# Performance work log

Hardware: AMD Instinct MI355X
Metric: run time of the kernel (lower is better)

Reference implementation:

```python
import jax, jax.numpy as jnp
import numpy as np
from jax.scipy.stats import norm

N_TOK, D_MODEL, N_EXP, N_SEL = 16384, 4096, 16, 4
NOISE_EPS = 0.01
LOSS_LAMBDA = 0.01


def setup_inputs() -> dict:
    key = jax.random.key(0)
    kx, k1, k2, kn, kz = jax.random.split(key, 5)
    x = jax.random.normal(kx, (N_TOK, D_MODEL), dtype=jnp.float32)
    w1 = jax.random.normal(k1, (N_EXP, D_MODEL), dtype=jnp.float32) * 0.02
    w2 = jax.random.normal(k2, (N_EXP, N_EXP), dtype=jnp.float32) * 0.02
    wn = jax.random.normal(kn, (N_EXP, D_MODEL), dtype=jnp.float32) * 0.02
    noise = jax.random.normal(kz, (N_TOK, N_EXP), dtype=jnp.float32)
    return {"x": x, "w1": w1, "w2": w2, "wn": wn, "noise": noise}


def _cv_squared(v, eps=1e-10):
    # torch .var() is unbiased (ddof=1)
    return jnp.var(v, ddof=1) / (jnp.mean(v) ** 2 + eps)


def reference(x, w1, w2, wn, noise):
    # MLP gate: Linear(D->E, no bias) -> tanh -> Linear(E->E, no bias)
    logits_gate = jnp.einsum("te,fe->tf", jnp.tanh(jnp.einsum("td,ed->te", x, w1)), w2)
    noise_control = jax.nn.softplus(jnp.einsum("td,ed->te", x, wn)) + NOISE_EPS
    logits_noise = noise * noise_control
    logits = logits_gate + logits_noise  # [T, E]

    m = min(N_SEL + 1, N_EXP)  # k+1 values for threshold computation
    top_logits, top_indices = jax.lax.top_k(logits, m)  # [T, m]
    top_k_logits = top_logits[:, :N_SEL]
    top_k_indices = top_indices[:, :N_SEL]
    top_k_scores = jax.nn.softmax(top_k_logits, axis=1)  # [T, k]

    # importance: scatter top-k scores back to dense [T, E]
    rows = jnp.arange(N_TOK)[:, None]
    scores_filtered = jnp.zeros_like(logits).at[rows, top_k_indices].set(top_k_scores)
    importance = scores_filtered.sum(0)  # [E]

    # load: smooth estimator via Normal CDF (faithful to source, which
    # compares logits_noise against the in/out thresholds)
    threshold_if_in = top_logits[:, N_SEL:N_SEL + 1]       # (k+1)-th top value, [T,1]
    threshold_if_out = top_logits[:, N_SEL - 1:N_SEL]      # k-th top value, [T,1]
    is_in = logits_noise > threshold_if_in
    prob_if_in = norm.cdf((logits_gate - threshold_if_in) / noise_control)
    prob_if_out = norm.cdf((logits_gate - threshold_if_out) / noise_control)
    prob = jnp.where(is_in, prob_if_in, prob_if_out)
    load = prob.sum(0)  # [E]

    gate_loss = LOSS_LAMBDA * (_cv_squared(importance) + _cv_squared(load))
    return top_k_indices, top_k_scores, gate_loss
```

## Files before the change

kernel.cpp:

```cpp
#include <hip/hip_runtime.h>
#include <math.h>

#define N_TOK   16384
#define D_MODEL 4096
#define N_EXP   16
#define N_SEL   4
#define WELEM   (N_EXP * D_MODEL)

typedef __bf16 bf16x8 __attribute__((ext_vector_type(8)));
typedef float  f32x4  __attribute__((ext_vector_type(4)));

#define MFMA(a, b, c) __builtin_amdgcn_mfma_f32_16x16x32_bf16((a), (b), (c), 0, 0, 0)
#define AS1 __attribute__((address_space(1)))
#define AS3 __attribute__((address_space(3)))

__global__ __launch_bounds__(256) void wprep_kernel(const float* __restrict__ w1,
                                                    const float* __restrict__ wn,
                                                    __bf16* __restrict__ wbuf)
{
    const int i = blockIdx.x * 256 + threadIdx.x;
    {
        const float v = w1[i];
        const __bf16 h = (__bf16)v;  const float r1 = v - (float)h;
        const __bf16 m = (__bf16)r1; const float r2 = r1 - (float)m;
        wbuf[i] = h; wbuf[WELEM + i] = m; wbuf[2 * WELEM + i] = (__bf16)r2;
    }
    {
        const float v = wn[i];
        const __bf16 h = (__bf16)v;  const float r1 = v - (float)h;
        const __bf16 m = (__bf16)r1; const float r2 = r1 - (float)m;
        wbuf[3 * WELEM + i] = h; wbuf[4 * WELEM + i] = m; wbuf[5 * WELEM + i] = (__bf16)r2;
    }
}

__device__ __forceinline__ void stage_load(const float* __restrict__ x,
                                           float4* xs, int buf, int w, int l,
                                           int t0, int kbase)
{
    #pragma unroll
    for (int j = 0; j < 8; ++j) {
        const int tl     = j * 2 + (l >> 5);
        const int k4slot = l & 31;
        const int k4data = k4slot ^ tl;
        const float* g = x + (size_t)(t0 + w * 16 + tl) * D_MODEL + kbase + k4data * 4;
        float4* lbase = xs + buf * 2048 + w * 512 + j * 64;
        __builtin_amdgcn_global_load_lds((const AS1 void*)(const void*)g,
                                         (AS3 void*)(void*)lbase, 16, 0, 0);
    }
}

__device__ __forceinline__ void split3(const float4 a, const float4 b,
                                       bf16x8& h, bf16x8& m, bf16x8& lo)
{
    const float v[8] = {a.x, a.y, a.z, a.w, b.x, b.y, b.z, b.w};
    #pragma unroll
    for (int j = 0; j < 8; ++j) {
        const __bf16 hh = (__bf16)v[j]; const float r1 = v[j] - (float)hh;
        const __bf16 mm = (__bf16)r1;   const float r2 = r1 - (float)mm;
        h[j] = hh; m[j] = mm; lo[j] = (__bf16)r2;
    }
}

__global__ __launch_bounds__(256, 2) void gate_kernel(
    const float* __restrict__ x, const __bf16* __restrict__ wbuf,
    const float* __restrict__ w2, const float* __restrict__ noise,
    float* __restrict__ out, float* __restrict__ g_imp, float* __restrict__ g_load)
{
    __shared__ float4 xs[4096];
    __shared__ float dsum[4][16][33];
    __shared__ float s_imp[N_EXP], s_ld[N_EXP];

    const int tid = threadIdx.x;
    const int l   = tid & 63;
    const int w   = tid >> 6;
    const int ml  = l & 15;
    const int q   = l >> 4;
    const int t0  = blockIdx.x * 64;

    const __bf16* w1h = wbuf;
    const __bf16* w1m = wbuf + WELEM;
    const __bf16* w1l = wbuf + 2 * WELEM;
    const __bf16* wnh = wbuf + 3 * WELEM;
    const __bf16* wnm = wbuf + 4 * WELEM;
    const __bf16* wnl = wbuf + 5 * WELEM;
    const int woff = ml * D_MODEL + q * 8;

    f32x4 c1 = {0.f, 0.f, 0.f, 0.f};
    f32x4 c2 = {0.f, 0.f, 0.f, 0.f};

    stage_load(x, xs, 0, w, l, t0, 0);
    if (tid < N_EXP) { s_imp[tid] = 0.f; s_ld[tid] = 0.f; }
    __syncthreads();

    for (int s = 0; s < 32; ++s) {
        if (s < 31) stage_load(x, xs, (s + 1) & 1, w, l, t0, (s + 1) * 128);

        const int kbase = s * 128;
        const int xb    = (s & 1) * 2048 + w * 512 + ml * 32;
        #pragma unroll
        for (int step = 0; step < 4; ++step) {
            const int kq = step * 8 + q * 2;
            const float4 va = xs[xb + (kq ^ ml)];
            const float4 vb = xs[xb + ((kq + 1) ^ ml)];
            bf16x8 xh, xm, xl;
            split3(va, vb, xh, xm, xl);

            const int wo = woff + kbase + step * 32;
            const bf16x8 a1h = *(const bf16x8*)(w1h + wo);
            const bf16x8 a1m = *(const bf16x8*)(w1m + wo);
            const bf16x8 a1l = *(const bf16x8*)(w1l + wo);
            const bf16x8 a2h = *(const bf16x8*)(wnh + wo);
            const bf16x8 a2m = *(const bf16x8*)(wnm + wo);
            const bf16x8 a2l = *(const bf16x8*)(wnl + wo);

            c1 = MFMA(a1h, xh, c1); c1 = MFMA(a1h, xm, c1); c1 = MFMA(a1m, xh, c1);
            c1 = MFMA(a1h, xl, c1); c1 = MFMA(a1l, xh, c1); c1 = MFMA(a1m, xm, c1);
            c2 = MFMA(a2h, xh, c2); c2 = MFMA(a2h, xm, c2); c2 = MFMA(a2m, xh, c2);
            c2 = MFMA(a2h, xl, c2); c2 = MFMA(a2l, xh, c2); c2 = MFMA(a2m, xm, c2);
        }
        __syncthreads();
    }

    #pragma unroll
    for (int r = 0; r < 4; ++r) {
        dsum[w][ml][q * 4 + r]      = c1[r];
        dsum[w][ml][16 + q * 4 + r] = c2[r];
    }
    __syncthreads();

    if (ml == l) {
        const int t = t0 + w * 16 + ml;
        float dot[32];
        #pragma unroll
        for (int e = 0; e < 32; ++e) dot[e] = dsum[w][ml][e];

        float th[N_EXP], nc[N_EXP];
        #pragma unroll
        for (int e = 0; e < N_EXP; ++e) th[e] = tanhf(dot[e]);
        #pragma unroll
        for (int e = 0; e < N_EXP; ++e) {
            const float v = dot[N_EXP + e];
            nc[e] = fmaxf(v, 0.f) + log1pf(expf(-fabsf(v))) + 0.01f;
        }

        float lg[N_EXP];
        #pragma unroll
        for (int f = 0; f < N_EXP; ++f) {
            float s = 0.f;
            #pragma unroll
            for (int e = 0; e < N_EXP; ++e) s = fmaf(th[e], w2[f * 16 + e], s);
            lg[f] = s;
        }

        float ln[N_EXP], v[N_EXP];
        {
            const float4* nz = (const float4*)(noise + (size_t)t * 16);
            const float4 n0 = nz[0], n1 = nz[1], n2 = nz[2], n3 = nz[3];
            const float nzv[16] = {n0.x, n0.y, n0.z, n0.w, n1.x, n1.y, n1.z, n1.w,
                                   n2.x, n2.y, n2.z, n2.w, n3.x, n3.y, n3.z, n3.w};
            #pragma unroll
            for (int e = 0; e < N_EXP; ++e) {
                ln[e] = nzv[e] * nc[e];
                v[e]  = lg[e] + ln[e];
            }
        }

        float tv[5]; int ti[5];
        #pragma unroll
        for (int j = 0; j < 5; ++j) {
            float best = -INFINITY; int bi = 0;
            #pragma unroll
            for (int e = 0; e < N_EXP; ++e) {
                bool taken = false;
                #pragma unroll
                for (int jj = 0; jj < 5; ++jj)
                    if (jj < j) taken = taken || (ti[jj] == e);
                if (!taken && v[e] > best) { best = v[e]; bi = e; }
            }
            tv[j] = best; ti[j] = bi;
        }

        const float mx = tv[0];
        float ex[4], ssum = 0.f;
        #pragma unroll
        for (int j = 0; j < 4; ++j) { ex[j] = expf(tv[j] - mx); ssum += ex[j]; }
        const float inv = 1.f / ssum;
        float sc[4];
        #pragma unroll
        for (int j = 0; j < 4; ++j) sc[j] = ex[j] * inv;

        #pragma unroll
        for (int j = 0; j < 4; ++j) atomicAdd(&s_imp[ti[j]], sc[j]);

        const float thr_in = tv[4], thr_out = tv[3];
        #pragma unroll
        for (int e = 0; e < N_EXP; ++e) {
            const bool  is_in = ln[e] > thr_in;
            const float thr   = is_in ? thr_in : thr_out;
            const float z     = (lg[e] - thr) / nc[e];
            const float prob  = 0.5f * (1.f + erff(z * 0.70710678118654752f));
            atomicAdd(&s_ld[e], prob);
        }

        ((float4*)out)[t] = make_float4((float)ti[0], (float)ti[1],
                                        (float)ti[2], (float)ti[3]);
        ((float4*)(out + N_TOK * N_SEL))[t] = make_float4(sc[0], sc[1], sc[2], sc[3]);
    }
    __syncthreads();
    if (tid < N_EXP)            atomicAdd(&g_imp[tid], s_imp[tid]);
    else if (tid < 2 * N_EXP)   atomicAdd(&g_load[tid - N_EXP], s_ld[tid - N_EXP]);
}

__global__ void loss_kernel(const float* __restrict__ g_imp,
                            const float* __restrict__ g_load,
                            float* __restrict__ out)
{
    if (threadIdx.x == 0 && blockIdx.x == 0) {
        double mi = 0.0, ml = 0.0;
        for (int e = 0; e < N_EXP; ++e) { mi += g_imp[e]; ml += g_load[e]; }
        mi /= N_EXP; ml /= N_EXP;
        double vi = 0.0, vl = 0.0;
        for (int e = 0; e < N_EXP; ++e) {
            const double di = g_imp[e] - mi;  vi += di * di;
            const double dl = g_load[e] - ml; vl += dl * dl;
        }
        vi /= (N_EXP - 1); vl /= (N_EXP - 1);
        const double ci = vi / (mi * mi + 1e-10);
        const double cl = vl / (ml * ml + 1e-10);
        out[N_TOK * N_SEL * 2] = (float)(0.01 * (ci + cl));
    }
}

extern "C" void kernel_launch(void* const* d_in, const int* in_sizes, int n_in,
                              void* d_out, int out_size, void* d_ws, size_t ws_size,
                              hipStream_t stream)
{
    const float* x     = (const float*)d_in[0];
    const float* w1    = (const float*)d_in[1];
    const float* w2    = (const float*)d_in[2];
    const float* wn    = (const float*)d_in[3];
    const float* noise = (const float*)d_in[4];
    float* out = (float*)d_out;

    __bf16* wbuf   = (__bf16*)d_ws;
    float*  g_imp  = (float*)((char*)d_ws + (1 << 20));
    float*  g_load = g_imp + N_EXP;

    hipMemsetAsync(g_imp, 0, 2 * N_EXP * sizeof(float), stream);

    wprep_kernel<<<WELEM / 256, 256, 0, stream>>>(w1, wn, wbuf);
    gate_kernel<<<N_TOK / 64, 256, 0, stream>>>(x, wbuf, w2, noise, out,
                                                g_imp, g_load);
    loss_kernel<<<1, 64, 0, stream>>>(g_imp, g_load, out);
}
```

Measured before the change: 457.1 us.

## Split-K the gate GEMM across blocks and move epilogue to separate kernel

```diff
diff --git a/kernel.cpp b/kernel.cpp
--- a/kernel.cpp
+++ b/kernel.cpp
@@ -6,13 +6,14 @@
 #define N_EXP   16
 #define N_SEL   4
 #define WELEM   (N_EXP * D_MODEL)
+#define KSPLIT  8
+#define KRANGE  (D_MODEL / KSPLIT)
+#define NSTEP   (KRANGE / 32)
 
 typedef __bf16 bf16x8 __attribute__((ext_vector_type(8)));
 typedef float  f32x4  __attribute__((ext_vector_type(4)));
 
 #define MFMA(a, b, c) __builtin_amdgcn_mfma_f32_16x16x32_bf16((a), (b), (c), 0, 0, 0)
-#define AS1 __attribute__((address_space(1)))
-#define AS3 __attribute__((address_space(3)))
 
 __global__ __launch_bounds__(256) void wprep_kernel(const float* __restrict__ w1,
                                                     const float* __restrict__ wn,
@@ -33,22 +34,6 @@
     }
 }
 
-__device__ __forceinline__ void stage_load(const float* __restrict__ x,
-                                           float4* xs, int buf, int w, int l,
-                                           int t0, int kbase)
-{
-    #pragma unroll
-    for (int j = 0; j < 8; ++j) {
-        const int tl     = j * 2 + (l >> 5);
-        const int k4slot = l & 31;
-        const int k4data = k4slot ^ tl;
-        const float* g = x + (size_t)(t0 + w * 16 + tl) * D_MODEL + kbase + k4data * 4;
-        float4* lbase = xs + buf * 2048 + w * 512 + j * 64;
-        __builtin_amdgcn_global_load_lds((const AS1 void*)(const void*)g,
-                                         (AS3 void*)(void*)lbase, 16, 0, 0);
-    }
-}
-
 __device__ __forceinline__ void split3(const float4 a, const float4 b,
                                        bf16x8& h, bf16x8& m, bf16x8& lo)
 {
@@ -61,154 +46,174 @@
     }
 }
 
-__global__ __launch_bounds__(256, 2) void gate_kernel(
+__global__ __launch_bounds__(256, 4) void gemm_kernel(
     const float* __restrict__ x, const __bf16* __restrict__ wbuf,
-    const float* __restrict__ w2, const float* __restrict__ noise,
-    float* __restrict__ out, float* __restrict__ g_imp, float* __restrict__ g_load)
-{
-    __shared__ float4 xs[4096];
-    __shared__ float dsum[4][16][33];
-    __shared__ float s_imp[N_EXP], s_ld[N_EXP];
-
+    float* __restrict__ dots)
+{
     const int tid = threadIdx.x;
     const int l   = tid & 63;
     const int w   = tid >> 6;
     const int ml  = l & 15;
     const int q   = l >> 4;
-    const int t0  = blockIdx.x * 64;
-
-    const __bf16* w1h = wbuf;
-    const __bf16* w1m = wbuf + WELEM;
-    const __bf16* w1l = wbuf + 2 * WELEM;
-    const __bf16* wnh = wbuf + 3 * WELEM;
-    const __bf16* wnm = wbuf + 4 * WELEM;
-    const __bf16* wnl = wbuf + 5 * WELEM;
-    const int woff = ml * D_MODEL + q * 8;
+    const int tb  = blockIdx.x >> 3;
+    const int ks  = blockIdx.x & 7;
+    const int kbase = ks * KRANGE;
+    const int trow  = tb * 64 + w * 16 + ml;
+
+    const __bf16* wp[6] = {wbuf,             wbuf + WELEM,     wbuf + 2 * WELEM,
+                           wbuf + 3 * WELEM, wbuf + 4 * WELEM, wbuf + 5 * WELEM};
+
+    const size_t xoff = (size_t)trow * D_MODEL + kbase + q * 8;
+    const int    woff = ml * D_MODEL + kbase + q * 8;
 
     f32x4 c1 = {0.f, 0.f, 0.f, 0.f};
     f32x4 c2 = {0.f, 0.f, 0.f, 0.f};
 
-    stage_load(x, xs, 0, w, l, t0, 0);
+    float4 xa[2], xb[2];
+    bf16x8 wr[2][6];
+
+    xa[0] = *(const float4*)(x + xoff);
+    xb[0] = *(const float4*)(x + xoff + 4);
+    #pragma unroll
+    for (int a = 0; a < 6; ++a) wr[0][a] = *(const bf16x8*)(wp[a] + woff);
+
+    #pragma unroll
+    for (int s = 0; s < NSTEP; ++s) {
+        const int cur = s & 1, nxt = cur ^ 1;
+        if (s + 1 < NSTEP) {
+            const int ko = (s + 1) * 32;
+            xa[nxt] = *(const float4*)(x + xoff + ko);
+            xb[nxt] = *(const float4*)(x + xoff + ko + 4);
+            #pragma unroll
+            for (int a = 0; a < 6; ++a)
+                wr[nxt][a] = *(const bf16x8*)(wp[a] + woff + ko);
+        }
+
+        bf16x8 xh, xm, xl;
+        split3(xa[cur], xb[cur], xh, xm, xl);
+
+        c1 = MFMA(wr[cur][0], xh, c1); c1 = MFMA(wr[cur][0], xm, c1);
+        c1 = MFMA(wr[cur][1], xh, c1); c1 = MFMA(wr[cur][0], xl, c1);
+        c1 = MFMA(wr[cur][2], xh, c1); c1 = MFMA(wr[cur][1], xm, c1);
+        c2 = MFMA(wr[cur][3], xh, c2); c2 = MFMA(wr[cur][3], xm, c2);
+        c2 = MFMA(wr[cur][4], xh, c2); c2 = MFMA(wr[cur][3], xl, c2);
+        c2 = MFMA(wr[cur][5], xh, c2); c2 = MFMA(wr[cur][4], xm, c2);
+    }
+
+    float* dst = dots + ((size_t)ks * N_TOK + trow) * 32 + q * 4;
+    *(float4*)(dst)      = make_float4(c1[0], c1[1], c1[2], c1[3]);
+    *(float4*)(dst + 16) = make_float4(c2[0], c2[1], c2[2], c2[3]);
+}
+
+__global__ __launch_bounds__(256) void epilogue_kernel(
+    const float* __restrict__ dots, const float* __restrict__ w2,
+    const float* __restrict__ noise, float* __restrict__ out,
+    float* __restrict__ g_imp, float* __restrict__ g_load)
+{
+    __shared__ float s_imp[N_EXP];
+    __shared__ float s_ld[N_EXP];
+    const int tid = threadIdx.x;
     if (tid < N_EXP) { s_imp[tid] = 0.f; s_ld[tid] = 0.f; }
     __syncthreads();
 
-    for (int s = 0; s < 32; ++s) {
-        if (s < 31) stage_load(x, xs, (s + 1) & 1, w, l, t0, (s + 1) * 128);
-
-        const int kbase = s * 128;
-        const int xb    = (s & 1) * 2048 + w * 512 + ml * 32;
-        #pragma unroll
-        for (int step = 0; step < 4; ++step) {
-            const int kq = step * 8 + q * 2;
-            const float4 va = xs[xb + (kq ^ ml)];
-            const float4 vb = xs[xb + ((kq + 1) ^ ml)];
-            bf16x8 xh, xm, xl;
-            split3(va, vb, xh, xm, xl);
-
-            const int wo = woff + kbase + step * 32;
-            const bf16x8 a1h = *(const bf16x8*)(w1h + wo);
-            const bf16x8 a1m = *(const bf16x8*)(w1m + wo);
-            const bf16x8 a1l = *(const bf16x8*)(w1l + wo);
-            const bf16x8 a2h = *(const bf16x8*)(wnh + wo);
-            const bf16x8 a2m = *(const bf16x8*)(wnm + wo);
-            const bf16x8 a2l = *(const bf16x8*)(wnl + wo);
-
-            c1 = MFMA(a1h, xh, c1); c1 = MFMA(a1h, xm, c1); c1 = MFMA(a1m, xh, c1);
-            c1 = MFMA(a1h, xl, c1); c1 = MFMA(a1l, xh, c1); c1 = MFMA(a1m, xm, c1);
-            c2 = MFMA(a2h, xh, c2); c2 = MFMA(a2h, xm, c2); c2 = MFMA(a2m, xh, c2);
-            c2 = MFMA(a2h, xl, c2); c2 = MFMA(a2l, xh, c2); c2 = MFMA(a2m, xm, c2);
-        }
-        __syncthreads();
-    }
-
-    #pragma unroll
-    for (int r = 0; r < 4; ++r) {
-        dsum[w][ml][q * 4 + r]      = c1[r];
-        dsum[w][ml][16 + q * 4 + r] = c2[r];
-    }
+    const int t = blockIdx.x * 256 + tid;
+
+    float4 a[8];
+    #pragma unroll
+    for (int j = 0; j < 8; ++j)
+        a[j] = ((const float4*)dots)[(size_t)t * 8 + j];
+    #pragma unroll
+    for (int ds = 1; ds < KSPLIT; ++ds) {
+        #pragma unroll
+        for (int j = 0; j < 8; ++j) {
+            float4 b = ((const float4*)dots)[((size_t)ds * N_TOK + t) * 8 + j];
+            a[j].x += b.x; a[j].y += b.y; a[j].z += b.z; a[j].w += b.w;
+        }
+    }
+    float dot[32];
+    #pragma unroll
+    for (int j = 0; j < 8; ++j) {
+        dot[4 * j + 0] = a[j].x; dot[4 * j + 1] = a[j].y;
+        dot[4 * j + 2] = a[j].z; dot[4 * j + 3] = a[j].w;
+    }
+
+    float th[N_EXP], nc[N_EXP];
+    #pragma unroll
+    for (int e = 0; e < N_EXP; ++e) th[e] = tanhf(dot[e]);
+    #pragma unroll
+    for (int e = 0; e < N_EXP; ++e) {
+        const float v = dot[N_EXP + e];
+        nc[e] = fmaxf(v, 0.f) + log1pf(expf(-fabsf(v))) + 0.01f;
+    }
+
+    float lg[N_EXP];
+    #pragma unroll
+    for (int f = 0; f < N_EXP; ++f) {
+        float s = 0.f;
+        #pragma unroll
+        for (int e = 0; e < N_EXP; ++e) s = fmaf(th[e], w2[f * 16 + e], s);
+        lg[f] = s;
+    }
+
+    float ln[N_EXP], v[N_EXP];
+    {
+        const float4* nz = (const float4*)(noise + (size_t)t * 16);
+        const float4 n0 = nz[0], n1 = nz[1], n2 = nz[2], n3 = nz[3];
+        const float nzv[16] = {n0.x, n0.y, n0.z, n0.w, n1.x, n1.y, n1.z, n1.w,
+                               n2.x, n2.y, n2.z, n2.w, n3.x, n3.y, n3.z, n3.w};
+        #pragma unroll
+        for (int e = 0; e < N_EXP; ++e) {
+            ln[e] = nzv[e] * nc[e];
+            v[e]  = lg[e] + ln[e];
+        }
+    }
+
+    float tv[5]; int ti[5];
+    #pragma unroll
+    for (int j = 0; j < 5; ++j) {
+        float best = -INFINITY; int bi = 0;
+        #pragma unroll
+        for (int e = 0; e < N_EXP; ++e) {
+            bool taken = false;
+            #pragma unroll
+            for (int jj = 0; jj < 5; ++jj)
+                if (jj < j) taken = taken || (ti[jj] == e);
+            if (!taken && v[e] > best) { best = v[e]; bi = e; }
+        }
+        tv[j] = best; ti[j] = bi;
+    }
+
+    const float mx = tv[0];
+    float ex[4], ssum = 0.f;
+    #pragma unroll
+    for (int j = 0; j < 4; ++j) { ex[j] = expf(tv[j] - mx); ssum += ex[j]; }
+    const float inv = 1.f / ssum;
+    float sc[4];
+    #pragma unroll
+    for (int j = 0; j < 4; ++j) sc[j] = ex[j] * inv;
+
+    #pragma unroll
+    for (int j = 0; j < 4; ++j) atomicAdd(&s_imp[ti[j]], sc[j]);
+
+    const float thr_in = tv[4], thr_out = tv[3];
+    #pragma unroll
+    for (int e = 0; e < N_EXP; ++e) {
+        const bool  is_in = ln[e] > thr_in;
+        const float thr   = is_in ? thr_in : thr_out;
+        const float z     = (lg[e] - thr) / nc[e];
+        const float prob  = 0.5f * (1.f + erff(z * 0.70710678118654752f));
+        atomicAdd(&s_ld[e], prob);
+    }
+
+    ((float4*)out)[t] = make_float4((float)ti[0], (float)ti[1],
+                                    (float)ti[2], (float)ti[3]);
+    ((float4*)(out + N_TOK * N_SEL))[t] = make_float4(sc[0], sc[1], sc[2], sc[3]);
+
     __syncthreads();
-
-    if (ml == l) {
-        const int t = t0 + w * 16 + ml;
-        float dot[32];
-        #pragma unroll
-        for (int e = 0; e < 32; ++e) dot[e] = dsum[w][ml][e];
-
-        float th[N_EXP], nc[N_EXP];
-        #pragma unroll
-        for (int e = 0; e < N_EXP; ++e) th[e] = tanhf(dot[e]);
-        #pragma unroll
-        for (int e = 0; e < N_EXP; ++e) {
-            const float v = dot[N_EXP + e];
-            nc[e] = fmaxf(v, 0.f) + log1pf(expf(-fabsf(v))) + 0.01f;
-        }
-
-        float lg[N_EXP];
-        #pragma unroll
-        for (int f = 0; f < N_EXP; ++f) {
-            float s = 0.f;
-            #pragma unroll
-            for (int e = 0; e < N_EXP; ++e) s = fmaf(th[e], w2[f * 16 + e], s);
-            lg[f] = s;
-        }
-
-        float ln[N_EXP], v[N_EXP];
-        {
-            const float4* nz = (const float4*)(noise + (size_t)t * 16);
-            const float4 n0 = nz[0], n1 = nz[1], n2 = nz[2], n3 = nz[3];
-            const float nzv[16] = {n0.x, n0.y, n0.z, n0.w, n1.x, n1.y, n1.z, n1.w,
-                                   n2.x, n2.y, n2.z, n2.w, n3.x, n3.y, n3.z, n3.w};
-            #pragma unroll
-            for (int e = 0; e < N_EXP; ++e) {
-                ln[e] = nzv[e] * nc[e];
-                v[e]  = lg[e] + ln[e];
-            }
-        }
-
-        float tv[5]; int ti[5];
-        #pragma unroll
-        for (int j = 0; j < 5; ++j) {
-            float best = -INFINITY; int bi = 0;
-            #pragma unroll
-            for (int e = 0; e < N_EXP; ++e) {
-                bool taken = false;
-                #pragma unroll
-                for (int jj = 0; jj < 5; ++jj)
-                    if (jj < j) taken = taken || (ti[jj] == e);
-                if (!taken && v[e] > best) { best = v[e]; bi = e; }
-            }
-            tv[j] = best; ti[j] = bi;
-        }
-
-        const float mx = tv[0];
-        float ex[4], ssum = 0.f;
-        #pragma unroll
-        for (int j = 0; j < 4; ++j) { ex[j] = expf(tv[j] - mx); ssum += ex[j]; }
-        const float inv = 1.f / ssum;
-        float sc[4];
-        #pragma unroll
-        for (int j = 0; j < 4; ++j) sc[j] = ex[j] * inv;
-
-        #pragma unroll
-        for (int j = 0; j < 4; ++j) atomicAdd(&s_imp[ti[j]], sc[j]);
-
-        const float thr_in = tv[4], thr_out = tv[3];
-        #pragma unroll
-        for (int e = 0; e < N_EXP; ++e) {
-            const bool  is_in = ln[e] > thr_in;
-            const float thr   = is_in ? thr_in : thr_out;
-            const float z     = (lg[e] - thr) / nc[e];
-            const float prob  = 0.5f * (1.f + erff(z * 0.70710678118654752f));
-            atomicAdd(&s_ld[e], prob);
-        }
-
-        ((float4*)out)[t] = make_float4((float)ti[0], (float)ti[1],
-                                        (float)ti[2], (float)ti[3]);
-        ((float4*)(out + N_TOK * N_SEL))[t] = make_float4(sc[0], sc[1], sc[2], sc[3]);
-    }
-    __syncthreads();
-    if (tid < N_EXP)            atomicAdd(&g_imp[tid], s_imp[tid]);
-    else if (tid < 2 * N_EXP)   atomicAdd(&g_load[tid - N_EXP], s_ld[tid - N_EXP]);
+    if (tid < N_EXP) {
+        atomicAdd(&g_imp[tid], s_imp[tid]);
+        atomicAdd(&g_load[tid], s_ld[tid]);
+    }
 }
 
 __global__ void loss_kernel(const float* __restrict__ g_imp,
@@ -245,11 +250,13 @@
     __bf16* wbuf   = (__bf16*)d_ws;
     float*  g_imp  = (float*)((char*)d_ws + (1 << 20));
     float*  g_load = g_imp + N_EXP;
+    float*  dots   = (float*)((char*)d_ws + (2 << 20));
 
     hipMemsetAsync(g_imp, 0, 2 * N_EXP * sizeof(float), stream);
 
     wprep_kernel<<<WELEM / 256, 256, 0, stream>>>(w1, wn, wbuf);
-    gate_kernel<<<N_TOK / 64, 256, 0, stream>>>(x, wbuf, w2, noise, out,
-                                                g_imp, g_load);
+    gemm_kernel<<<256 * KSPLIT, 256, 0, stream>>>(x, wbuf, dots);
+    epilogue_kernel<<<N_TOK / 256, 256, 0, stream>>>(dots, w2, noise, out,
+                                                     g_imp, g_load);
     loss_kernel<<<1, 64, 0, stream>>>(g_imp, g_load, out);
 }
```

After: 490.3 us. +7.3%, slower.
